# Optimization experiments

Measured on AMD Instinct MI355X. Metric: run time of the kernel, lower is better.

Reference implementation:

```python
import jax, jax.numpy as jnp
import numpy as np

V, D, B, S, T, MAXLEN = 32000, 256, 4, 512, 256, 512


def _gru(x, Wih, Whh, bih, bhh):
    """torch-style GRU over x:[B,L,Din] -> [B,L,D]. Weight rows ordered [r,z,n]."""
    Dh = Whh.shape[1]
    xW = x @ Wih.T + bih  # [B,L,3D] precompute input projections

    def step(h, xw):
        hW = h @ Whh.T + bhh
        xr, xz, xn = jnp.split(xw, 3, axis=-1)
        hr, hz, hn = jnp.split(hW, 3, axis=-1)
        r = jax.nn.sigmoid(xr + hr)
        z = jax.nn.sigmoid(xz + hz)
        n = jnp.tanh(xn + r * hn)
        h = (1.0 - z) * n + z * h
        return h, h

    h0 = jnp.zeros((x.shape[0], Dh), x.dtype)
    _, ys = jax.lax.scan(step, h0, jnp.swapaxes(xW, 0, 1))
    return jnp.swapaxes(ys, 0, 1)


def setup_inputs() -> dict:
    key = jax.random.key(0)
    ks = jax.random.split(key, 24)

    def n(k, shape, scale=0.02):
        return (jax.random.normal(k, shape, jnp.float32) * scale).astype(jnp.float32)

    inp = {
        "src": jax.random.randint(ks[0], (B, S), 0, V),
        "tgt": jax.random.randint(ks[1], (B, T), 0, V),
        "emb": n(ks[2], (V, D)),
        "pos": n(ks[3], (MAXLEN, D)),
        # encoder forward direction
        "ef_wih": n(ks[4], (3 * D, D)), "ef_whh": n(ks[5], (3 * D, D)),
        "ef_bih": n(ks[6], (3 * D,)), "ef_bhh": n(ks[7], (3 * D,)),
        # encoder backward direction
        "eb_wih": n(ks[8], (3 * D, D)), "eb_whh": n(ks[9], (3 * D, D)),
        "eb_bih": n(ks[10], (3 * D,)), "eb_bhh": n(ks[11], (3 * D,)),
        # decoder
        "d_wih": n(ks[12], (3 * D, D)), "d_whh": n(ks[13], (3 * D, D)),
        "d_bih": n(ks[14], (3 * D,)), "d_bhh": n(ks[15], (3 * D,)),
        "Wq": n(ks[16], (D, D)),
        "Wk": n(ks[17], (D, 2 * D)),
        "Wgen": n(ks[18], (V, 3 * D)), "bgen": n(ks[19], (V,)),
        "Wgate": n(ks[20], (1, 3 * D)), "bgate": n(ks[21], (1,)),
    }
    return inp


def reference(src, tgt, emb, pos,
              ef_wih, ef_whh, ef_bih, ef_bhh,
              eb_wih, eb_whh, eb_bih, eb_bhh,
              d_wih, d_whh, d_bih, d_bhh,
              Wq, Wk, Wgen, bgen, Wgate, bgate):
    b, s = src.shape
    t = tgt.shape[1]
    d = emb.shape[1]
    v = emb.shape[0]

    src_emb = emb[src] + pos[:s][None]          # [B,S,D]
    enc_f = _gru(src_emb, ef_wih, ef_whh, ef_bih, ef_bhh)
    enc_b = _gru(src_emb[:, ::-1], eb_wih, eb_whh, eb_bih, eb_bhh)[:, ::-1]
    enc_out = jnp.concatenate([enc_f, enc_b], axis=-1)  # [B,S,2D]

    tgt_emb = emb[tgt] + pos[:t][None]
    dec_out = _gru(tgt_emb, d_wih, d_whh, d_bih, d_bhh)  # [B,T,D]

    Q = dec_out @ Wq.T                           # [B,T,D]
    K = enc_out @ Wk.T                           # [B,S,D]
    scores = jnp.einsum('btd,bsd->bts', Q, K) / jnp.sqrt(jnp.asarray(d, jnp.float32))
    pos_probs = jax.nn.softmax(scores, axis=-1)  # [B,T,S]

    # copy distribution: scatter attention mass into vocab buckets (== one_hot bmm)
    P_copy = jnp.zeros((b, t, v), pos_probs.dtype).at[
        jnp.arange(b)[:, None, None],
        jnp.arange(t)[None, :, None],
        src[:, None, :],
    ].add(pos_probs)

    ctx_f = jnp.einsum('bts,bsd->btd', pos_probs, enc_f)
    ctx_b = jnp.einsum('bts,bsd->btd', pos_probs, enc_b)
    combined = jnp.concatenate([dec_out, ctx_f, ctx_b], axis=-1)  # [B,T,3D]

    P_gen = jax.nn.softmax(combined @ Wgen.T + bgen, axis=-1)     # [B,T,V]
    gate = jax.nn.sigmoid(combined @ Wgate.T + bgate)             # [B,T,1]
    return gate * P_gen + (1.0 - gate) * P_copy
```

## Files before the change

kernel.cpp:

```cpp
#include <hip/hip_runtime.h>
#include <hip/hip_bf16.h>
#include <math.h>

#define VV   32000
#define DIM  256
#define BB   4
#define SS   512
#define TT   256
#define D2   512
#define D3   768

typedef __attribute__((ext_vector_type(8))) short s16x8;
typedef __attribute__((ext_vector_type(4))) float f32x4;

__device__ __forceinline__ float sigmoidf_(float x) { return 1.0f / (1.0f + __expf(-x)); }
__device__ __forceinline__ float tanhf_(float x) {
    float e2 = __expf(2.0f * x);
    return (e2 - 1.0f) / (e2 + 1.0f);
}
__device__ __forceinline__ short f2bf(float f) {
    unsigned u = __float_as_uint(f);
    u += 0x7FFFu + ((u >> 16) & 1u);
    return (short)(u >> 16);
}

#define BAR_LGKM() asm volatile("s_waitcnt lgkmcnt(0)\n\ts_barrier" ::: "memory")

__global__ __launch_bounds__(256) void k_embed(const int* __restrict__ src,
                                               const int* __restrict__ tgt,
                                               const float* __restrict__ emb,
                                               const float* __restrict__ pos,
                                               float* __restrict__ src_emb,
                                               float* __restrict__ tgt_emb) {
    int i = blockIdx.x * 256 + threadIdx.x;
    const int nS = BB * SS * DIM;
    if (i < nS) {
        int d = i & (DIM - 1);
        int s = (i >> 8) & (SS - 1);
        int b = i >> 17;
        src_emb[i] = emb[(size_t)src[b * SS + s] * DIM + d] + pos[s * DIM + d];
    } else {
        int j = i - nS;
        int d = j & (DIM - 1);
        int t = (j >> 8) & (TT - 1);
        int b = j >> 16;
        tgt_emb[j] = emb[(size_t)tgt[b * TT + t] * DIM + d] + pos[t * DIM + d];
    }
}

struct GDesc {
    const float* A; int lda;
    const float* Bt; int ldb;
    const float* bias;
    float* C; int ldc;
    int M, N;
};

#define BMM 128
#define BNN 128
#define BKK 8

__global__ __launch_bounds__(256) void k_gemmb(GDesc d0, GDesc d1, GDesc d2) {
    GDesc d = (blockIdx.z == 0) ? d0 : ((blockIdx.z == 1) ? d1 : d2);
    int brow = blockIdx.y * BMM, bcol = blockIdx.x * BNN;
    if (brow >= d.M || bcol >= d.N) return;

    __shared__ float As[BKK][BMM + 4];
    __shared__ float Bs[BKK][BNN + 4];
    const int K = d.lda;
    int tid = threadIdx.x;
    int tx = tid & 15, ty = tid >> 4;
    float acc[8][8];
#pragma unroll
    for (int i = 0; i < 8; i++)
#pragma unroll
        for (int j = 0; j < 8; j++) acc[i][j] = 0.0f;

    int lr = tid >> 1;
    int lk = (tid & 1) * 4;
    for (int k0 = 0; k0 < K; k0 += BKK) {
        float4 a4 = *(const float4*)&d.A[(size_t)(brow + lr) * d.lda + k0 + lk];
        float4 b4 = *(const float4*)&d.Bt[(size_t)(bcol + lr) * d.ldb + k0 + lk];
        As[lk + 0][lr] = a4.x; As[lk + 1][lr] = a4.y; As[lk + 2][lr] = a4.z; As[lk + 3][lr] = a4.w;
        Bs[lk + 0][lr] = b4.x; Bs[lk + 1][lr] = b4.y; Bs[lk + 2][lr] = b4.z; Bs[lk + 3][lr] = b4.w;
        __syncthreads();
#pragma unroll
        for (int kk = 0; kk < BKK; kk++) {
            float4 a0 = *(const float4*)&As[kk][ty * 8];
            float4 a1 = *(const float4*)&As[kk][ty * 8 + 4];
            float4 b0 = *(const float4*)&Bs[kk][tx * 8];
            float4 b1 = *(const float4*)&Bs[kk][tx * 8 + 4];
            float av[8] = {a0.x, a0.y, a0.z, a0.w, a1.x, a1.y, a1.z, a1.w};
            float bv[8] = {b0.x, b0.y, b0.z, b0.w, b1.x, b1.y, b1.z, b1.w};
#pragma unroll
            for (int i = 0; i < 8; i++)
#pragma unroll
                for (int j = 0; j < 8; j++) acc[i][j] += av[i] * bv[j];
        }
        __syncthreads();
    }

    float bv0[8];
#pragma unroll
    for (int j = 0; j < 8; j++) bv0[j] = d.bias ? d.bias[bcol + tx * 8 + j] : 0.0f;

#pragma unroll
    for (int i = 0; i < 8; i++) {
        size_t row = brow + ty * 8 + i;
        float4 c0 = make_float4(acc[i][0] + bv0[0], acc[i][1] + bv0[1],
                                acc[i][2] + bv0[2], acc[i][3] + bv0[3]);
        float4 c1 = make_float4(acc[i][4] + bv0[4], acc[i][5] + bv0[5],
                                acc[i][6] + bv0[6], acc[i][7] + bv0[7]);
        *(float4*)&d.C[row * d.ldc + bcol + tx * 8] = c0;
        *(float4*)&d.C[row * d.ldc + bcol + tx * 8 + 4] = c1;
    }
}

__global__ __launch_bounds__(512, 2) void k_gru(const float* __restrict__ ef_x,
                                                const float* __restrict__ eb_x,
                                                const float* __restrict__ d_x,
                                                const float* __restrict__ ef_whh, const float* __restrict__ ef_bhh,
                                                const float* __restrict__ eb_whh, const float* __restrict__ eb_bhh,
                                                const float* __restrict__ d_whh, const float* __restrict__ d_bhh,
                                                float* __restrict__ enc_out,
                                                float* __restrict__ dec_out) {
    __shared__ __align__(16) short hb[2][4 * 256];

    int tid = threadIdx.x;
    int dir = blockIdx.x;
    const float *xw, *Whh, *bhh;
    int L;
    if (dir == 0)      { xw = ef_x; Whh = ef_whh; bhh = ef_bhh; L = SS; }
    else if (dir == 1) { xw = eb_x; Whh = eb_whh; bhh = eb_bhh; L = SS; }
    else               { xw = d_x;  Whh = d_whh;  bhh = d_bhh;  L = TT; }

    const int wv = tid >> 6;
    const int lane = tid & 63;
    const int jj = lane & 15;
    const int hi = lane >> 4;
    const int b = hi;

    if (tid < 256) {
        f32x4 z = {0.f, 0.f, 0.f, 0.f};
        *(f32x4*)((char*)hb + tid * 16) = z;
    }

    s16x8 wf[3][2][8];
#pragma unroll
    for (int g = 0; g < 3; ++g)
#pragma unroll
        for (int t = 0; t < 2; ++t) {
            const int nrow = g * 256 + wv * 32 + t * 16 + jj;
            const float* wp = Whh + (size_t)nrow * 256 + hi * 8;
#pragma unroll
            for (int sk = 0; sk < 8; ++sk) {
                float4 w0 = *(const float4*)(wp + sk * 32);
                float4 w1 = *(const float4*)(wp + sk * 32 + 4);
                s16x8 v;
                v[0] = f2bf(w0.x); v[1] = f2bf(w0.y); v[2] = f2bf(w0.z); v[3] = f2bf(w0.w);
                v[4] = f2bf(w1.x); v[5] = f2bf(w1.y); v[6] = f2bf(w1.z); v[7] = f2bf(w1.w);
                wf[g][t][sk] = v;
            }
        }

    const int j0 = wv * 32 + jj, j1 = j0 + 16;
    const float br0 = bhh[j0], bz0 = bhh[256 + j0], bn0 = bhh[512 + j0];
    const float br1 = bhh[j1], bz1 = bhh[256 + j1], bn1 = bhh[512 + j1];

    const int arow = jj >> 2;
    const int abase = arow * 512 + hi * 16;
    const int aswz = arow << 4;
    const int wo0 = (b * 512 + 2 * j0) ^ (b << 4);
    const int wo1 = (b * 512 + 2 * j1) ^ (b << 4);

    const int s0 = (dir == 1) ? (L - 1) : 0;
    const int sst = (dir == 1) ? -1 : 1;
    const float* xq = xw + ((size_t)b * L + s0) * D3 + j0;
    float* op;
    int ostride;
    if (dir == 2) { op = dec_out + ((size_t)b * TT + s0) * DIM + j0; ostride = sst * DIM; }
    else          { op = enc_out + ((size_t)b * SS + s0) * D2 + (dir == 1 ? DIM : 0) + j0; ostride = sst * D2; }
    const int xstride = sst * D3;

    float c0 = xq[0], c1 = xq[256], c2 = xq[512], c3 = xq[16], c4 = xq[272], c5 = xq[528];

    float h0 = 0.f, h1 = 0.f;
    int cur = 0;
    __syncthreads();

    for (int st = 0; st < L; ++st) {
        xq += xstride;
        float n0 = xq[0], n1 = xq[256], n2 = xq[512], n3 = xq[16], n4 = xq[272], n5 = xq[528];

        const char* hcur = (const char*)hb + cur * 2048;
        f32x4 a00 = {0.f, 0.f, 0.f, 0.f}, a01 = a00, a10 = a00, a11 = a00, a20 = a00, a21 = a00;
#pragma unroll
        for (int sk = 0; sk < 8; ++sk) {
            s16x8 af = *(const s16x8*)(hcur + ((abase + 64 * sk) ^ aswz));
            a00 = __builtin_amdgcn_mfma_f32_16x16x32_bf16(af, wf[0][0][sk], a00, 0, 0, 0);
            a01 = __builtin_amdgcn_mfma_f32_16x16x32_bf16(af, wf[0][1][sk], a01, 0, 0, 0);
            a10 = __builtin_amdgcn_mfma_f32_16x16x32_bf16(af, wf[1][0][sk], a10, 0, 0, 0);
            a11 = __builtin_amdgcn_mfma_f32_16x16x32_bf16(af, wf[1][1][sk], a11, 0, 0, 0);
            a20 = __builtin_amdgcn_mfma_f32_16x16x32_bf16(af, wf[2][0][sk], a20, 0, 0, 0);
            a21 = __builtin_amdgcn_mfma_f32_16x16x32_bf16(af, wf[2][1][sk], a21, 0, 0, 0);
        }

        float r0 = sigmoidf_(c0 + a00[0] + br0);
        float z0 = sigmoidf_(c1 + a10[0] + bz0);
        float nn0 = tanhf_(c2 + r0 * (a20[0] + bn0));
        h0 = (1.f - z0) * nn0 + z0 * h0;
        float r1 = sigmoidf_(c3 + a01[0] + br1);
        float z1 = sigmoidf_(c4 + a11[0] + bz1);
        float nn1 = tanhf_(c5 + r1 * (a21[0] + bn1));
        h1 = (1.f - z1) * nn1 + z1 * h1;

        char* hnxt = (char*)hb + (cur ^ 1) * 2048;
        *(short*)(hnxt + wo0) = f2bf(h0);
        *(short*)(hnxt + wo1) = f2bf(h1);
        op[0] = h0;
        op[16] = h1;
        BAR_LGKM();

        cur ^= 1;
        c0 = n0; c1 = n1; c2 = n2; c3 = n3; c4 = n4; c5 = n5;
        op += ostride;
    }
}

__global__ __launch_bounds__(256) void k_attn(const float* __restrict__ Qb,
                                              const float* __restrict__ Kb,
                                              const float* __restrict__ enc_out,
                                              const float* __restrict__ dec_out,
                                              const float* __restrict__ Wgate,
                                              const float* __restrict__ bgate,
                                              float* __restrict__ probs,
                                              short* __restrict__ cmb,
                                              float* __restrict__ gate) {
    __shared__ float q[DIM];
    __shared__ float sc[SS];
    __shared__ float red[256];
    int row = blockIdx.x;
    int b = row >> 8;
    int tid = threadIdx.x;

    q[tid] = Qb[(size_t)row * DIM + tid];
    __syncthreads();

    const float scale = 0.0625f;
#pragma unroll
    for (int h = 0; h < 2; h++) {
        int s2 = tid + h * 256;
        const float* kr = Kb + ((size_t)b * SS + s2) * DIM;
        float acc = 0.0f;
        for (int k = 0; k < DIM; k += 4) {
            float4 k4 = *(const float4*)&kr[k];
            acc += k4.x * q[k] + k4.y * q[k + 1] + k4.z * q[k + 2] + k4.w * q[k + 3];
        }
        sc[s2] = acc * scale;
    }
    __syncthreads();

    red[tid] = fmaxf(sc[tid], sc[tid + 256]);
    __syncthreads();
    for (int o = 128; o > 0; o >>= 1) {
        if (tid < o) red[tid] = fmaxf(red[tid], red[tid + o]);
        __syncthreads();
    }
    float m = red[0];
    __syncthreads();

    float e0 = __expf(sc[tid] - m), e1 = __expf(sc[tid + 256] - m);
    sc[tid] = e0; sc[tid + 256] = e1;
    red[tid] = e0 + e1;
    __syncthreads();
    for (int o = 128; o > 0; o >>= 1) {
        if (tid < o) red[tid] += red[tid + o];
        __syncthreads();
    }
    float inv = 1.0f / red[0];
    __syncthreads();

    sc[tid] *= inv; sc[tid + 256] *= inv;
    probs[(size_t)row * SS + tid] = sc[tid];
    probs[(size_t)row * SS + tid + 256] = sc[tid + 256];
    __syncthreads();

    float accf = 0.0f, accb = 0.0f;
    const float* ep = enc_out + (size_t)b * SS * D2 + tid;
    for (int s = 0; s < SS; s++) {
        float p = sc[s];
        accf += p * ep[(size_t)s * D2];
        accb += p * ep[(size_t)s * D2 + DIM];
    }
    float dv = dec_out[(size_t)row * DIM + tid];
    cmb[(size_t)row * D3 + tid] = f2bf(dv);
    cmb[(size_t)row * D3 + DIM + tid] = f2bf(accf);
    cmb[(size_t)row * D3 + 2 * DIM + tid] = f2bf(accb);

    red[tid] = dv * Wgate[tid] + accf * Wgate[DIM + tid] + accb * Wgate[2 * DIM + tid];
    __syncthreads();
    for (int o = 128; o > 0; o >>= 1) {
        if (tid < o) red[tid] += red[tid + o];
        __syncthreads();
    }
    if (tid == 0) gate[row] = sigmoidf_(red[0] + bgate[0]);
}

__global__ __launch_bounds__(512) void k_gen(const short* __restrict__ A,
                                             const float* __restrict__ Bw,
                                             const float* __restrict__ bias,
                                             float* __restrict__ C,
                                             float* __restrict__ rowsum) {
    __shared__ __align__(16) short As[256 * 32];
    __shared__ __align__(16) short Bs[128 * 32];
    int tid = threadIdx.x;
    int lane = tid & 63, wv = tid >> 6;
    int wm = wv >> 1, wn = wv & 1;
    int brow = blockIdx.y * 256, bcol = blockIdx.x * 128;
    f32x4 acc[4][4];
#pragma unroll
    for (int i = 0; i < 4; i++)
#pragma unroll
        for (int j = 0; j < 4; j++) acc[i][j] = (f32x4){0.f, 0.f, 0.f, 0.f};

    const int ca0 = tid, ca1 = tid + 512, cb = tid;
    const int ll = lane & 15, lh = lane >> 4;

    for (int k0 = 0; k0 < D3; k0 += 32) {
        s16x8 va0 = *(const s16x8*)&A[(size_t)(brow + (ca0 >> 2)) * D3 + k0 + (ca0 & 3) * 8];
        s16x8 va1 = *(const s16x8*)&A[(size_t)(brow + (ca1 >> 2)) * D3 + k0 + (ca1 & 3) * 8];
        const float* bp = &Bw[(size_t)(bcol + (cb >> 2)) * D3 + k0 + (cb & 3) * 8];
        float4 b0 = *(const float4*)bp;
        float4 b1 = *(const float4*)(bp + 4);
        s16x8 vb;
        vb[0] = f2bf(b0.x); vb[1] = f2bf(b0.y); vb[2] = f2bf(b0.z); vb[3] = f2bf(b0.w);
        vb[4] = f2bf(b1.x); vb[5] = f2bf(b1.y); vb[6] = f2bf(b1.z); vb[7] = f2bf(b1.w);

        __syncthreads();
        *(s16x8*)&As[ca0 * 8] = va0;
        *(s16x8*)&As[ca1 * 8] = va1;
        *(s16x8*)&Bs[cb * 8] = vb;
        __syncthreads();

        s16x8 af[4], bf[4];
#pragma unroll
        for (int mt = 0; mt < 4; ++mt)
            af[mt] = *(const s16x8*)&As[(wm * 64 + mt * 16 + ll) * 32 + lh * 8];
#pragma unroll
        for (int nt = 0; nt < 4; ++nt)
            bf[nt] = *(const s16x8*)&Bs[(wn * 64 + nt * 16 + ll) * 32 + lh * 8];
#pragma unroll
        for (int mt = 0; mt < 4; ++mt)
#pragma unroll
            for (int nt = 0; nt < 4; ++nt)
                acc[mt][nt] = __builtin_amdgcn_mfma_f32_16x16x32_bf16(af[mt], bf[nt], acc[mt][nt], 0, 0, 0);
    }

#pragma unroll
    for (int nt = 0; nt < 4; ++nt) {
        float bv = bias[bcol + wn * 64 + nt * 16 + ll];
#pragma unroll
        for (int mt = 0; mt < 4; ++mt)
#pragma unroll
            for (int q = 0; q < 4; ++q) acc[mt][nt][q] += bv;
    }

#pragma unroll
    for (int mt = 0; mt < 4; ++mt) {
        int row = brow + wm * 64 + mt * 16 + lh * 4;
#pragma unroll
        for (int nt = 0; nt < 4; ++nt) {
            int col = bcol + wn * 64 + nt * 16 + ll;
#pragma unroll
            for (int q = 0; q < 4; ++q)
                C[(size_t)(row + q) * VV + col] = acc[mt][nt][q];
        }
    }

#pragma unroll
    for (int mt = 0; mt < 4; ++mt) {
#pragma unroll
        for (int q = 0; q < 4; ++q) {
            float se = __expf(acc[mt][0][q]) + __expf(acc[mt][1][q]) +
                       __expf(acc[mt][2][q]) + __expf(acc[mt][3][q]);
#pragma unroll
            for (int off = 1; off < 16; off <<= 1)
                se += __shfl_xor(se, off);
            if (ll == 0) {
                int row = brow + wm * 64 + mt * 16 + lh * 4 + q;
                atomicAdd(&rowsum[row], se);
            }
        }
    }
}

__global__ __launch_bounds__(256) void k_final(const float* __restrict__ gate,
                                               const float* __restrict__ rowsum,
                                               float* __restrict__ out) {
    size_t i4 = (size_t)blockIdx.x * 256 + threadIdx.x;
    size_t base = i4 * 4;
    int row = (int)(base / VV);
    float inv = gate[row] / rowsum[row];
    float4 l = *(const float4*)&out[base];
    l.x = __expf(l.x) * inv;
    l.y = __expf(l.y) * inv;
    l.z = __expf(l.z) * inv;
    l.w = __expf(l.w) * inv;
    *(float4*)&out[base] = l;
}

__global__ __launch_bounds__(256) void k_scatter(const int* __restrict__ src,
                                                 const float* __restrict__ probs,
                                                 const float* __restrict__ gate,
                                                 float* __restrict__ out) {
    int i = blockIdx.x * 256 + threadIdx.x;
    int s = i & (SS - 1);
    int row = i >> 9;
    int b = row >> 8;
    float g = gate[row];
    float val = (1.0f - g) * probs[(size_t)row * SS + s];
    int col = src[b * SS + s];
    atomicAdd(&out[(size_t)row * VV + col], val);
}

extern "C" void kernel_launch(void* const* d_in, const int* in_sizes, int n_in,
                              void* d_out, int out_size, void* d_ws, size_t ws_size,
                              hipStream_t stream) {
    const int*   src    = (const int*)d_in[0];
    const int*   tgt    = (const int*)d_in[1];
    const float* emb    = (const float*)d_in[2];
    const float* pos    = (const float*)d_in[3];
    const float* ef_wih = (const float*)d_in[4];
    const float* ef_whh = (const float*)d_in[5];
    const float* ef_bih = (const float*)d_in[6];
    const float* ef_bhh = (const float*)d_in[7];
    const float* eb_wih = (const float*)d_in[8];
    const float* eb_whh = (const float*)d_in[9];
    const float* eb_bih = (const float*)d_in[10];
    const float* eb_bhh = (const float*)d_in[11];
    const float* d_wih  = (const float*)d_in[12];
    const float* d_whh  = (const float*)d_in[13];
    const float* d_bih  = (const float*)d_in[14];
    const float* d_bhh  = (const float*)d_in[15];
    const float* Wq     = (const float*)d_in[16];
    const float* Wk     = (const float*)d_in[17];
    const float* Wgen   = (const float*)d_in[18];
    const float* bgen   = (const float*)d_in[19];
    const float* Wgate  = (const float*)d_in[20];
    const float* bgate  = (const float*)d_in[21];
    float* out = (float*)d_out;
    float* ws  = (float*)d_ws;

    float* src_emb  = ws;
    float* tgt_emb  = src_emb + (size_t)BB * SS * DIM;
    float* ef_x     = tgt_emb + (size_t)BB * TT * DIM;
    float* eb_x     = ef_x + (size_t)BB * SS * D3;
    float* d_x      = eb_x + (size_t)BB * SS * D3;
    float* enc_out  = d_x + (size_t)BB * TT * D3;
    float* dec_out  = enc_out + (size_t)BB * SS * D2;
    float* Qb       = dec_out + (size_t)BB * TT * DIM;
    float* Kb       = Qb + (size_t)BB * TT * DIM;
    float* probs    = Kb + (size_t)BB * SS * DIM;
    short* cmb_bf   = (short*)(probs + (size_t)BB * TT * SS);
    float* gate     = (float*)(cmb_bf + (size_t)BB * TT * D3);
    float* rowsum   = gate + 1024;

    hipMemsetAsync(rowsum, 0, 1024 * sizeof(float), stream);

    k_embed<<<(BB * SS * DIM + BB * TT * DIM) / 256, 256, 0, stream>>>(
        src, tgt, emb, pos, src_emb, tgt_emb);

    {
        GDesc e0 = {src_emb, DIM, ef_wih, DIM, ef_bih, ef_x, D3, BB * SS, D3};
        GDesc e1 = {src_emb, DIM, eb_wih, DIM, eb_bih, eb_x, D3, BB * SS, D3};
        GDesc e2 = {tgt_emb, DIM, d_wih, DIM, d_bih, d_x, D3, BB * TT, D3};
        k_gemmb<<<dim3(D3 / BNN, BB * SS / BMM, 3), 256, 0, stream>>>(e0, e1, e2);
    }

    k_gru<<<3, 512, 0, stream>>>(ef_x, eb_x, d_x, ef_whh, ef_bhh, eb_whh, eb_bhh,
                                 d_whh, d_bhh, enc_out, dec_out);

    {
        GDesc q0 = {dec_out, DIM, Wq, DIM, nullptr, Qb, DIM, BB * TT, DIM};
        GDesc q1 = {enc_out, D2, Wk, D2, nullptr, Kb, DIM, BB * SS, DIM};
        k_gemmb<<<dim3(DIM / BNN, BB * SS / BMM, 2), 256, 0, stream>>>(q0, q1, q1);
    }

    k_attn<<<BB * TT, 256, 0, stream>>>(Qb, Kb, enc_out, dec_out, Wgate, bgate,
                                        probs, cmb_bf, gate);

    k_gen<<<dim3(VV / 128, (BB * TT) / 256), 512, 0, stream>>>(cmb_bf, Wgen, bgen, out, rowsum);

    k_final<<<(BB * TT * VV) / 1024, 256, 0, stream>>>(gate, rowsum, out);
    k_scatter<<<(BB * TT * SS) / 256, 256, 0, stream>>>(src, probs, gate, out);
}
```

Baseline: 1.186 ms.

## Double attention block threads and tweak GRU barrier scheduling priority

The attention kernel now runs 512 threads per row. Each thread computes one score, and the context accumulation is split over two halves of the source sequence, with the partial sums combined in shared memory. This halves the serial loop length per thread. The GRU recurrence loop also raises wave priority around its MFMA chain and wraps the barrier in sched_barriers, to keep the compiler from reordering work across the step barrier. The cost is more shared memory and one extra reduction step in attention.

Result: slower. 1.422 ms (+19.9%).

```diff
diff --git a/kernel.cpp b/kernel.cpp
--- a/kernel.cpp
+++ b/kernel.cpp
@@ -24,7 +24,12 @@
     return (short)(u >> 16);
 }
 
-#define BAR_LGKM() asm volatile("s_waitcnt lgkmcnt(0)\n\ts_barrier" ::: "memory")
+#define GRU_BAR() do {                                   \
+    __builtin_amdgcn_sched_barrier(0);                   \
+    asm volatile("s_waitcnt lgkmcnt(0)" ::);             \
+    __builtin_amdgcn_s_barrier();                        \
+    __builtin_amdgcn_sched_barrier(0);                   \
+} while (0)
 
 __global__ __launch_bounds__(256) void k_embed(const int* __restrict__ src,
                                                const int* __restrict__ tgt,
@@ -194,6 +199,7 @@
 
         const char* hcur = (const char*)hb + cur * 2048;
         f32x4 a00 = {0.f, 0.f, 0.f, 0.f}, a01 = a00, a10 = a00, a11 = a00, a20 = a00, a21 = a00;
+        __builtin_amdgcn_s_setprio(1);
 #pragma unroll
         for (int sk = 0; sk < 8; ++sk) {
             s16x8 af = *(const s16x8*)(hcur + ((abase + 64 * sk) ^ aswz));
@@ -204,6 +210,7 @@
             a20 = __builtin_amdgcn_mfma_f32_16x16x32_bf16(af, wf[2][0][sk], a20, 0, 0, 0);
             a21 = __builtin_amdgcn_mfma_f32_16x16x32_bf16(af, wf[2][1][sk], a21, 0, 0, 0);
         }
+        __builtin_amdgcn_s_setprio(0);
 
         float r0 = sigmoidf_(c0 + a00[0] + br0);
         float z0 = sigmoidf_(c1 + a10[0] + bz0);
@@ -219,7 +226,7 @@
         *(short*)(hnxt + wo1) = f2bf(h1);
         op[0] = h0;
         op[16] = h1;
-        BAR_LGKM();
+        GRU_BAR();
 
         cur ^= 1;
         c0 = n0; c1 = n1; c2 = n2; c3 = n3; c4 = n4; c5 = n5;
@@ -227,7 +234,7 @@
     }
 }
 
-__global__ __launch_bounds__(256) void k_attn(const float* __restrict__ Qb,
+__global__ __launch_bounds__(512) void k_attn(const float* __restrict__ Qb,
                                               const float* __restrict__ Kb,
                                               const float* __restrict__ enc_out,
                                               const float* __restrict__ dec_out,
@@ -238,66 +245,75 @@
                                               float* __restrict__ gate) {
     __shared__ float q[DIM];
     __shared__ float sc[SS];
-    __shared__ float red[256];
+    __shared__ float red[512];
+    __shared__ float par[2][2][DIM];
     int row = blockIdx.x;
     int b = row >> 8;
     int tid = threadIdx.x;
 
-    q[tid] = Qb[(size_t)row * DIM + tid];
+    if (tid < DIM) q[tid] = Qb[(size_t)row * DIM + tid];
     __syncthreads();
 
     const float scale = 0.0625f;
-#pragma unroll
-    for (int h = 0; h < 2; h++) {
-        int s2 = tid + h * 256;
-        const float* kr = Kb + ((size_t)b * SS + s2) * DIM;
+    {
+        const float* kr = Kb + ((size_t)b * SS + tid) * DIM;
         float acc = 0.0f;
         for (int k = 0; k < DIM; k += 4) {
             float4 k4 = *(const float4*)&kr[k];
             acc += k4.x * q[k] + k4.y * q[k + 1] + k4.z * q[k + 2] + k4.w * q[k + 3];
         }
-        sc[s2] = acc * scale;
-    }
-    __syncthreads();
-
-    red[tid] = fmaxf(sc[tid], sc[tid + 256]);
-    __syncthreads();
-    for (int o = 128; o > 0; o >>= 1) {
+        sc[tid] = acc * scale;
+    }
+    __syncthreads();
+
+    red[tid] = sc[tid];
+    __syncthreads();
+    for (int o = 256; o > 0; o >>= 1) {
         if (tid < o) red[tid] = fmaxf(red[tid], red[tid + o]);
         __syncthreads();
     }
     float m = red[0];
     __syncthreads();
 
-    float e0 = __expf(sc[tid] - m), e1 = __expf(sc[tid + 256] - m);
-    sc[tid] = e0; sc[tid + 256] = e1;
-    red[tid] = e0 + e1;
-    __syncthreads();
-    for (int o = 128; o > 0; o >>= 1) {
+    float e0 = __expf(sc[tid] - m);
+    sc[tid] = e0;
+    red[tid] = e0;
+    __syncthreads();
+    for (int o = 256; o > 0; o >>= 1) {
         if (tid < o) red[tid] += red[tid + o];
         __syncthreads();
     }
     float inv = 1.0f / red[0];
     __syncthreads();
 
-    sc[tid] *= inv; sc[tid + 256] *= inv;
+    sc[tid] *= inv;
     probs[(size_t)row * SS + tid] = sc[tid];
-    probs[(size_t)row * SS + tid + 256] = sc[tid + 256];
-    __syncthreads();
-
-    float accf = 0.0f, accb = 0.0f;
-    const float* ep = enc_out + (size_t)b * SS * D2 + tid;
-    for (int s = 0; s < SS; s++) {
-        float p = sc[s];
-        accf += p * ep[(size_t)s * D2];
-        accb += p * ep[(size_t)s * D2 + DIM];
-    }
-    float dv = dec_out[(size_t)row * DIM + tid];
-    cmb[(size_t)row * D3 + tid] = f2bf(dv);
-    cmb[(size_t)row * D3 + DIM + tid] = f2bf(accf);
-    cmb[(size_t)row * D3 + 2 * DIM + tid] = f2bf(accb);
-
-    red[tid] = dv * Wgate[tid] + accf * Wgate[DIM + tid] + accb * Wgate[2 * DIM + tid];
+    __syncthreads();
+
+    {
+        int d = tid & 255, sh = tid >> 8;
+        float accf = 0.0f, accb = 0.0f;
+        const float* ep = enc_out + ((size_t)b * SS + sh * 256) * D2 + d;
+        const float* pp = &sc[sh * 256];
+        for (int s = 0; s < 256; s++) {
+            float p = pp[s];
+            accf += p * ep[(size_t)s * D2];
+            accb += p * ep[(size_t)s * D2 + DIM];
+        }
+        par[sh][0][d] = accf;
+        par[sh][1][d] = accb;
+    }
+    __syncthreads();
+
+    if (tid < DIM) {
+        float af = par[0][0][tid] + par[1][0][tid];
+        float ab = par[0][1][tid] + par[1][1][tid];
+        float dv = dec_out[(size_t)row * DIM + tid];
+        cmb[(size_t)row * D3 + tid] = f2bf(dv);
+        cmb[(size_t)row * D3 + DIM + tid] = f2bf(af);
+        cmb[(size_t)row * D3 + 2 * DIM + tid] = f2bf(ab);
+        red[tid] = dv * Wgate[tid] + af * Wgate[DIM + tid] + ab * Wgate[2 * DIM + tid];
+    }
     __syncthreads();
     for (int o = 128; o > 0; o >>= 1) {
         if (tid < o) red[tid] += red[tid + o];
@@ -486,7 +502,7 @@
         k_gemmb<<<dim3(DIM / BNN, BB * SS / BMM, 2), 256, 0, stream>>>(q0, q1, q1);
     }
 
-    k_attn<<<BB * TT, 256, 0, stream>>>(Qb, Kb, enc_out, dec_out, Wgate, bgate,
+    k_attn<<<BB * TT, 512, 0, stream>>>(Qb, Kb, enc_out, dec_out, Wgate, bgate,
                                         probs, cmb_bf, gate);
 
     k_gen<<<dim3(VV / 128, (BB * TT) / 256), 512, 0, stream>>>(cmb_bf, Wgen, bgen, out, rowsum);
```
